# Performance work log

Hardware: AMD Instinct MI355X
Metric: run time of the kernel (lower is better)

Reference implementation:

```python
import jax, jax.numpy as jnp
import numpy as np

N_NODES = 100000
N_EDGES = 1600000
IN_FEATS = 64
HIDDEN = 64
NUM_CLASSES = 2


def setup_inputs() -> dict:
    key = jax.random.key(0)
    ks = jax.random.split(key, 9)
    feat = jax.random.normal(ks[0], (N_NODES, IN_FEATS), dtype=jnp.float32)
    src = jax.random.randint(ks[1], (N_EDGES,), 0, N_NODES, dtype=jnp.int64) if jax.config.jax_enable_x64 else jax.random.randint(ks[1], (N_EDGES,), 0, N_NODES).astype(jnp.int32)
    dst = jax.random.randint(ks[2], (N_EDGES,), 0, N_NODES).astype(src.dtype)
    s_in = 1.0 / np.sqrt(IN_FEATS)
    s_e = 1.0 / np.sqrt(2 * HIDDEN)
    s_o = 1.0 / np.sqrt(HIDDEN)
    W_in = jax.random.uniform(ks[3], (IN_FEATS, HIDDEN), jnp.float32, -s_in, s_in)
    b_in = jax.random.uniform(ks[4], (HIDDEN,), jnp.float32, -s_in, s_in)
    W_edge = jax.random.uniform(ks[5], (2 * HIDDEN, 1), jnp.float32, -s_e, s_e)
    b_edge = jax.random.uniform(ks[6], (1,), jnp.float32, -s_e, s_e)
    W_out = jax.random.uniform(ks[7], (HIDDEN, NUM_CLASSES), jnp.float32, -s_o, s_o)
    b_out = jax.random.uniform(ks[8], (NUM_CLASSES,), jnp.float32, -s_o, s_o)
    return {"feat": feat, "src": src, "dst": dst, "W_in": W_in, "b_in": b_in,
            "W_edge": W_edge, "b_edge": b_edge, "W_out": W_out, "b_out": b_out}


def reference(feat, src, dst, W_in, b_in, W_edge, b_edge, W_out, b_out):
    # input node MLP: [N, in] @ [in, H]
    h = feat @ W_in + b_in  # [N, H]
    # edge function: sigmoid(Linear(cat(h_src, h_dst))) -- split concat to avoid [E, 2H] buffer
    hu = h[src]  # [E, H]
    hv = h[dst]  # [E, H]
    W_u, W_v = W_edge[:HIDDEN], W_edge[HIDDEN:]  # each [H, 1]
    w = jax.nn.sigmoid(hu @ W_u + hv @ W_v + b_edge)  # [E, 1]
    # message = h_src * w, reduce = sum over incoming edges at dst
    msgs = hu * w  # [E, H]
    agg = jax.ops.segment_sum(msgs, dst, num_segments=N_NODES)  # [N, H]
    # DGL UDF-reduce semantics: zero in-degree nodes keep previous h
    deg = jax.ops.segment_sum(jnp.ones((dst.shape[0],), dtype=jnp.float32), dst, num_segments=N_NODES)
    h_new = jnp.where(deg[:, None] > 0, agg, h)
    return h_new @ W_out + b_out  # [N, num_classes]
```

## Files before the change

### kernel.cpp

```cpp
#include <hip/hip_runtime.h>
#include <math.h>

#define N_NODES 100000
#define N_EDGES 1600000

#define BK_LOG 8
#define BKW 256
#define NBK ((N_NODES + BKW - 1) / BKW)
#define CAPB 4864
#define UNS4 3

#define GS 800
#define EPS (N_EDGES / GS)
#define EPS4 (EPS / 4)

#define NT_BLOCKS ((N_NODES + 63) / 64)

__global__ __launch_bounds__(256) void prep_kernel(
    const float* __restrict__ feat,
    const float* __restrict__ W_in,
    const float* __restrict__ b_in,
    const float* __restrict__ W_edge,
    const float* __restrict__ W_out,
    const int*   __restrict__ src,
    const int*   __restrict__ dst,
    int* __restrict__ cursor,
    int* __restrict__ ework,
    float4* __restrict__ nodeT)
{
    const int tid = threadIdx.x;

    if ((int)blockIdx.x >= NT_BLOCKS) {
        __shared__ int hist[NBK];
        __shared__ int base[NBK];
        for (int i = tid; i < NBK; i += 256) hist[i] = 0;
        __syncthreads();

        const int4* src4 = (const int4*)src;
        const int4* dst4 = (const int4*)dst;
        const int   b40  = ((blockIdx.x - NT_BLOCKS) * EPS) >> 2;

        int bb[8], rr[8], pk[8];
        #pragma unroll
        for (int j = 0; j < 2; ++j) {
            const int o4 = j * 256 + tid;
            if (o4 < EPS4) {
                const int4 d4 = dst4[b40 + o4];
                const int4 s4 = src4[b40 + o4];
                const int dv[4] = {d4.x, d4.y, d4.z, d4.w};
                const int sv[4] = {s4.x, s4.y, s4.z, s4.w};
                #pragma unroll
                for (int u = 0; u < 4; ++u) {
                    const int idx = j * 4 + u;
                    const int d = dv[u];
                    const int b = d >> BK_LOG;
                    bb[idx] = b;
                    rr[idx] = atomicAdd(&hist[b], 1);
                    pk[idx] = ((d & (BKW - 1)) << 17) | sv[u];
                }
            }
        }
        __syncthreads();

        for (int b = tid; b < NBK; b += 256) {
            const int c = hist[b];
            if (c) base[b] = atomicAdd(&cursor[b], c);
        }
        __syncthreads();

        #pragma unroll
        for (int j = 0; j < 2; ++j) {
            const int o4 = j * 256 + tid;
            if (o4 < EPS4) {
                #pragma unroll
                for (int u = 0; u < 4; ++u) {
                    const int idx = j * 4 + u;
                    ework[bb[idx] * CAPB + base[bb[idx]] + rr[idx]] = pk[idx];
                }
            }
        }
        return;
    }

    __shared__ float sP[64 * 4];
    __shared__ float sQ[64 * 4];
    __shared__ float sc[4];

    if (tid < 64) {
        sP[tid * 4 + 0] = W_edge[tid];
        sP[tid * 4 + 1] = W_out[tid * 2 + 0];
        sP[tid * 4 + 2] = W_out[tid * 2 + 1];
        sP[tid * 4 + 3] = W_edge[64 + tid];
    }
    __syncthreads();

    {
        const int k = tid >> 2, j = tid & 3;
        float q = 0.f;
        for (int m = 0; m < 64; ++m) q += W_in[k * 64 + m] * sP[m * 4 + j];
        sQ[k * 4 + j] = q;
        if (tid < 4) {
            float cc = 0.f;
            for (int m = 0; m < 64; ++m) cc += b_in[m] * sP[m * 4 + tid];
            sc[tid] = cc;
        }
    }
    __syncthreads();

    const int lane = tid & 63;
    const int wv   = tid >> 6;
    const int n    = blockIdx.x * 64 + wv * 16 + (lane >> 2);
    const int ks   = (lane & 3) << 4;

    float p0 = 0.f, p1 = 0.f, p2 = 0.f, p3 = 0.f;
    if (n < N_NODES) {
        const float* fr = feat + (size_t)n * 64 + ks;
        #pragma unroll
        for (int i4 = 0; i4 < 4; ++i4) {
            const float4 f = *(const float4*)(fr + i4 * 4);
            const float fv[4] = {f.x, f.y, f.z, f.w};
            #pragma unroll
            for (int u = 0; u < 4; ++u) {
                const float4 q = *(const float4*)&sQ[(ks + i4 * 4 + u) * 4];
                p0 += fv[u] * q.x;
                p1 += fv[u] * q.y;
                p2 += fv[u] * q.z;
                p3 += fv[u] * q.w;
            }
        }
    }
    #pragma unroll
    for (int off = 1; off <= 2; off <<= 1) {
        p0 += __shfl_xor(p0, off);
        p1 += __shfl_xor(p1, off);
        p2 += __shfl_xor(p2, off);
        p3 += __shfl_xor(p3, off);
    }
    if (n < N_NODES && (lane & 3) == 0)
        nodeT[n] = make_float4(p0 + sc[0], p1 + sc[1], p2 + sc[2], p3 + sc[3]);
}

__global__ __launch_bounds__(512) void sortagg_kernel(
    const int* __restrict__ ework,
    const int* __restrict__ cursor,
    const float4* __restrict__ nodeT,
    const float* __restrict__ b_edge,
    const float* __restrict__ b_out,
    float2* __restrict__ out)
{
    __shared__ int hist[BKW];
    __shared__ int sdata[BKW];
    __shared__ int sbase[BKW];
    __shared__ int ssorted[CAPB];

    const int b   = blockIdx.x;
    const int tid = threadIdx.x;

    if (tid < BKW) hist[tid] = 0;
    __syncthreads();

    const int cnt = min(cursor[b], CAPB);
    const int4* ew4 = (const int4*)(ework + b * CAPB);

    int4 vv[UNS4];
    int  rk[UNS4][4];
    #pragma unroll
    for (int j = 0; j < UNS4; ++j) {
        const int o = (j * 512 + tid) * 4;
        if (o < cnt) {
            const int4 v = ew4[j * 512 + tid];
            vv[j] = v;
            const int ve[4] = {v.x, v.y, v.z, v.w};
            #pragma unroll
            for (int u = 0; u < 4; ++u)
                if (o + u < cnt) rk[j][u] = atomicAdd(&hist[ve[u] >> 17], 1);
        }
    }
    __syncthreads();

    int own = 0;
    if (tid < BKW) { own = hist[tid]; sdata[tid] = own; }
    __syncthreads();
    for (int off = 1; off < BKW; off <<= 1) {
        int t = 0;
        if (tid < BKW && tid >= off) t = sdata[tid - off];
        __syncthreads();
        if (tid < BKW) sdata[tid] += t;
        __syncthreads();
    }
    if (tid < BKW) sbase[tid] = sdata[tid] - own;
    __syncthreads();

    #pragma unroll
    for (int j = 0; j < UNS4; ++j) {
        const int o = (j * 512 + tid) * 4;
        if (o < cnt) {
            const int4 v = vv[j];
            const int ve[4] = {v.x, v.y, v.z, v.w};
            #pragma unroll
            for (int u = 0; u < 4; ++u)
                if (o + u < cnt)
                    ssorted[sbase[ve[u] >> 17] + rk[j][u]] = ve[u] & 0x1FFFF;
        }
    }
    __syncthreads();

    const int sub = tid & 3;
    const float be  = b_edge[0];
    const float bo0 = b_out[0];
    const float bo1 = b_out[1];

    #pragma unroll
    for (int pass = 0; pass < 2; ++pass) {
        const int l = pass * 128 + (tid >> 2);
        const int n = b * BKW + l;

        float4 tn = make_float4(0.f, 0.f, 0.f, 0.f);
        if (n < N_NODES) tn = nodeT[n];
        const int   beg = sbase[l];
        const int   len = hist[l];
        const float Bn  = tn.w + be;

        float m0 = 0.f, m1 = 0.f;
        for (int i = sub; i < len; i += 4) {
            const int    s = ssorted[beg + i];
            const float4 t = nodeT[s];
            const float  w = 1.0f / (1.0f + __expf(-(t.x + Bn)));
            m0 += w * t.y;
            m1 += w * t.z;
        }
        m0 += __shfl_xor(m0, 1);
        m1 += __shfl_xor(m1, 1);
        m0 += __shfl_xor(m0, 2);
        m1 += __shfl_xor(m1, 2);

        if (sub == 0 && n < N_NODES) {
            const float o0 = (len ? m0 : tn.y) + bo0;
            const float o1 = (len ? m1 : tn.z) + bo1;
            out[n] = make_float2(o0, o1);
        }
    }
}

extern "C" void kernel_launch(void* const* d_in, const int* in_sizes, int n_in,
                              void* d_out, int out_size, void* d_ws, size_t ws_size,
                              hipStream_t stream) {
    const float* feat   = (const float*)d_in[0];
    const int*   src    = (const int*)d_in[1];
    const int*   dst    = (const int*)d_in[2];
    const float* W_in   = (const float*)d_in[3];
    const float* b_in   = (const float*)d_in[4];
    const float* W_edge = (const float*)d_in[5];
    const float* b_edge = (const float*)d_in[6];
    const float* W_out  = (const float*)d_in[7];
    const float* b_out  = (const float*)d_in[8];
    float2* out = (float2*)d_out;

    float4* nodeT  = (float4*)d_ws;
    int*    ework  = (int*)(nodeT + N_NODES);
    int*    cursor = ework + NBK * CAPB;

    hipMemsetAsync(cursor, 0, NBK * sizeof(int), stream);

    prep_kernel<<<NT_BLOCKS + GS, 256, 0, stream>>>(
        feat, W_in, b_in, W_edge, W_out, src, dst, cursor, ework, nodeT);
    sortagg_kernel<<<NBK, 512, 0, stream>>>(
        ework, cursor, nodeT, b_edge, b_out, out);
}
```

Baseline: 131.4 us.

## Replace per-bucket LDS sort with coarse buckets and shared-memory atomic aggregation

Buckets edges by destination in coarse 1024-node super-buckets instead of 256-node buckets, and removes the in-block counting sort. Each super-bucket is now processed by 8 blocks, and each block scans the whole edge list and keeps only the edges whose destination falls in its 128-node slice. Partial sums are accumulated with float atomics in shared memory. The bucketing blocks are moved to the front of the grid so they get scheduled first. This removes the histogram, scan and scatter work, but each edge is read 8 times, LDS atomics can contend, and float atomics make the summation order nondeterministic.

Result: slower. 148.3 us (+12.9%).

```diff
diff --git a/kernel.cpp b/kernel.cpp
--- a/kernel.cpp
+++ b/kernel.cpp
@@ -4,11 +4,10 @@
 #define N_NODES 100000
 #define N_EDGES 1600000
 
-#define BK_LOG 8
-#define BKW 256
-#define NBK ((N_NODES + BKW - 1) / BKW)
-#define CAPB 4864
-#define UNS4 3
+#define SB_LOG 10
+#define SBW 1024
+#define NSB ((N_NODES + SBW - 1) / SBW)
+#define CAP 18000
 
 #define GS 800
 #define EPS (N_EDGES / GS)
@@ -30,15 +29,15 @@
 {
     const int tid = threadIdx.x;
 
-    if ((int)blockIdx.x >= NT_BLOCKS) {
-        __shared__ int hist[NBK];
-        __shared__ int base[NBK];
-        for (int i = tid; i < NBK; i += 256) hist[i] = 0;
+    if ((int)blockIdx.x < GS) {
+        __shared__ int hist[NSB];
+        __shared__ int base[NSB];
+        for (int i = tid; i < NSB; i += 256) hist[i] = 0;
         __syncthreads();
 
         const int4* src4 = (const int4*)src;
         const int4* dst4 = (const int4*)dst;
-        const int   b40  = ((blockIdx.x - NT_BLOCKS) * EPS) >> 2;
+        const int   b40  = (blockIdx.x * EPS) >> 2;
 
         int bb[8], rr[8], pk[8];
         #pragma unroll
@@ -53,16 +52,16 @@
                 for (int u = 0; u < 4; ++u) {
                     const int idx = j * 4 + u;
                     const int d = dv[u];
-                    const int b = d >> BK_LOG;
+                    const int b = d >> SB_LOG;
                     bb[idx] = b;
                     rr[idx] = atomicAdd(&hist[b], 1);
-                    pk[idx] = ((d & (BKW - 1)) << 17) | sv[u];
+                    pk[idx] = ((d & (SBW - 1)) << 17) | sv[u];
                 }
             }
         }
         __syncthreads();
 
-        for (int b = tid; b < NBK; b += 256) {
+        for (int b = tid; b < NSB; b += 256) {
             const int c = hist[b];
             if (c) base[b] = atomicAdd(&cursor[b], c);
         }
@@ -75,7 +74,7 @@
                 #pragma unroll
                 for (int u = 0; u < 4; ++u) {
                     const int idx = j * 4 + u;
-                    ework[bb[idx] * CAPB + base[bb[idx]] + rr[idx]] = pk[idx];
+                    ework[bb[idx] * CAP + base[bb[idx]] + rr[idx]] = pk[idx];
                 }
             }
         }
@@ -84,7 +83,7 @@
 
     __shared__ float sP[64 * 4];
     __shared__ float sQ[64 * 4];
-    __shared__ float sc[4];
+    __shared__ float sc4[4];
 
     if (tid < 64) {
         sP[tid * 4 + 0] = W_edge[tid];
@@ -102,14 +101,14 @@
         if (tid < 4) {
             float cc = 0.f;
             for (int m = 0; m < 64; ++m) cc += b_in[m] * sP[m * 4 + tid];
-            sc[tid] = cc;
+            sc4[tid] = cc;
         }
     }
     __syncthreads();
 
     const int lane = tid & 63;
     const int wv   = tid >> 6;
-    const int n    = blockIdx.x * 64 + wv * 16 + (lane >> 2);
+    const int n    = (blockIdx.x - GS) * 64 + wv * 16 + (lane >> 2);
     const int ks   = (lane & 3) << 4;
 
     float p0 = 0.f, p1 = 0.f, p2 = 0.f, p3 = 0.f;
@@ -137,10 +136,10 @@
         p3 += __shfl_xor(p3, off);
     }
     if (n < N_NODES && (lane & 3) == 0)
-        nodeT[n] = make_float4(p0 + sc[0], p1 + sc[1], p2 + sc[2], p3 + sc[3]);
+        nodeT[n] = make_float4(p0 + sc4[0], p1 + sc4[1], p2 + sc4[2], p3 + sc4[3]);
 }
 
-__global__ __launch_bounds__(512) void sortagg_kernel(
+__global__ __launch_bounds__(256) void agg_kernel(
     const int* __restrict__ ework,
     const int* __restrict__ cursor,
     const float4* __restrict__ nodeT,
@@ -148,95 +147,60 @@
     const float* __restrict__ b_out,
     float2* __restrict__ out)
 {
-    __shared__ int hist[BKW];
-    __shared__ int sdata[BKW];
-    __shared__ int sbase[BKW];
-    __shared__ int ssorted[CAPB];
-
-    const int b   = blockIdx.x;
+    __shared__ float sB[128];
+    __shared__ float sm0[128];
+    __shared__ float sm1[128];
+    __shared__ int   spres[128];
+
+    const int bo  = blockIdx.x;
+    const int b   = bo >> 3;
+    const int oc  = bo & 7;
     const int tid = threadIdx.x;
-
-    if (tid < BKW) hist[tid] = 0;
-    __syncthreads();
-
-    const int cnt = min(cursor[b], CAPB);
-    const int4* ew4 = (const int4*)(ework + b * CAPB);
-
-    int4 vv[UNS4];
-    int  rk[UNS4][4];
-    #pragma unroll
-    for (int j = 0; j < UNS4; ++j) {
-        const int o = (j * 512 + tid) * 4;
-        if (o < cnt) {
-            const int4 v = ew4[j * 512 + tid];
-            vv[j] = v;
-            const int ve[4] = {v.x, v.y, v.z, v.w};
-            #pragma unroll
-            for (int u = 0; u < 4; ++u)
-                if (o + u < cnt) rk[j][u] = atomicAdd(&hist[ve[u] >> 17], 1);
-        }
-    }
-    __syncthreads();
-
-    int own = 0;
-    if (tid < BKW) { own = hist[tid]; sdata[tid] = own; }
-    __syncthreads();
-    for (int off = 1; off < BKW; off <<= 1) {
-        int t = 0;
-        if (tid < BKW && tid >= off) t = sdata[tid - off];
-        __syncthreads();
-        if (tid < BKW) sdata[tid] += t;
-        __syncthreads();
-    }
-    if (tid < BKW) sbase[tid] = sdata[tid] - own;
-    __syncthreads();
-
-    #pragma unroll
-    for (int j = 0; j < UNS4; ++j) {
-        const int o = (j * 512 + tid) * 4;
-        if (o < cnt) {
-            const int4 v = vv[j];
-            const int ve[4] = {v.x, v.y, v.z, v.w};
-            #pragma unroll
-            for (int u = 0; u < 4; ++u)
-                if (o + u < cnt)
-                    ssorted[sbase[ve[u] >> 17] + rk[j][u]] = ve[u] & 0x1FFFF;
-        }
-    }
-    __syncthreads();
-
-    const int sub = tid & 3;
-    const float be  = b_edge[0];
-    const float bo0 = b_out[0];
-    const float bo1 = b_out[1];
-
-    #pragma unroll
-    for (int pass = 0; pass < 2; ++pass) {
-        const int l = pass * 128 + (tid >> 2);
-        const int n = b * BKW + l;
-
-        float4 tn = make_float4(0.f, 0.f, 0.f, 0.f);
-        if (n < N_NODES) tn = nodeT[n];
-        const int   beg = sbase[l];
-        const int   len = hist[l];
-        const float Bn  = tn.w + be;
-
-        float m0 = 0.f, m1 = 0.f;
-        for (int i = sub; i < len; i += 4) {
-            const int    s = ssorted[beg + i];
-            const float4 t = nodeT[s];
-            const float  w = 1.0f / (1.0f + __expf(-(t.x + Bn)));
-            m0 += w * t.y;
-            m1 += w * t.z;
-        }
-        m0 += __shfl_xor(m0, 1);
-        m1 += __shfl_xor(m1, 1);
-        m0 += __shfl_xor(m0, 2);
-        m1 += __shfl_xor(m1, 2);
-
-        if (sub == 0 && n < N_NODES) {
-            const float o0 = (len ? m0 : tn.y) + bo0;
-            const float o1 = (len ? m1 : tn.z) + bo1;
+    const int nb  = b * SBW + oc * 128;
+
+    float fb0 = 0.f, fb1 = 0.f;
+    if (tid < 128) {
+        const int n = nb + tid;
+        float4 t = make_float4(0.f, 0.f, 0.f, 0.f);
+        if (n < N_NODES) t = nodeT[n];
+        sB[tid] = t.w;
+        fb0 = t.y; fb1 = t.z;
+        sm0[tid] = 0.f; sm1[tid] = 0.f; spres[tid] = 0;
+    }
+    __syncthreads();
+
+    const int cnt  = min(cursor[b], CAP);
+    const int cnt4 = (cnt + 3) >> 2;
+    const int4* ew4 = (const int4*)(ework + b * CAP);
+    const float be = b_edge[0];
+
+    for (int i = tid; i < cnt4; i += 256) {
+        const int4 v = ew4[i];
+        const int ve[4] = {v.x, v.y, v.z, v.w};
+        const int o0 = i * 4;
+        #pragma unroll
+        for (int u = 0; u < 4; ++u) {
+            if (o0 + u < cnt) {
+                const int p = ve[u];
+                if (((p >> 24) & 7) == oc) {
+                    const int dl = (p >> 17) & 127;
+                    const int s  = p & 0x1FFFF;
+                    const float4 t = nodeT[s];
+                    const float  w = 1.0f / (1.0f + __expf(-(t.x + be + sB[dl])));
+                    atomicAdd(&sm0[dl], w * t.y);
+                    atomicAdd(&sm1[dl], w * t.z);
+                    spres[dl] = 1;
+                }
+            }
+        }
+    }
+    __syncthreads();
+
+    if (tid < 128) {
+        const int n = nb + tid;
+        if (n < N_NODES) {
+            const float o0 = (spres[tid] ? sm0[tid] : fb0) + b_out[0];
+            const float o1 = (spres[tid] ? sm1[tid] : fb1) + b_out[1];
             out[n] = make_float2(o0, o1);
         }
     }
@@ -258,12 +222,12 @@
 
     float4* nodeT  = (float4*)d_ws;
     int*    ework  = (int*)(nodeT + N_NODES);
-    int*    cursor = ework + NBK * CAPB;
-
-    hipMemsetAsync(cursor, 0, NBK * sizeof(int), stream);
-
-    prep_kernel<<<NT_BLOCKS + GS, 256, 0, stream>>>(
+    int*    cursor = ework + NSB * CAP;
+
+    hipMemsetAsync(cursor, 0, NSB * sizeof(int), stream);
+
+    prep_kernel<<<GS + NT_BLOCKS, 256, 0, stream>>>(
         feat, W_in, b_in, W_edge, W_out, src, dst, cursor, ework, nodeT);
-    sortagg_kernel<<<NBK, 512, 0, stream>>>(
+    agg_kernel<<<NSB * 8, 256, 0, stream>>>(
         ework, cursor, nodeT, b_edge, b_out, out);
 }
```
